# Optimization experiments

Measured on AMD Instinct MI355X. Metric: run time of the kernel, lower is better.

## Reference

```python
import jax, jax.numpy as jnp
from jax import lax
import numpy as np


def setup_inputs() -> dict:
    B, P, L, H, T = 4, 160, 128, 768, 9
    rng = np.random.default_rng(0)
    sent_length = rng.integers(L // 2, L + 1, size=B)
    sent_length[0] = L  # ensure max length equals L (pad_packed total_length)
    p2w = np.zeros((B, L, P), dtype=bool)
    for bi in range(B):
        pos = 1  # skip [CLS]
        for w in range(int(sent_length[bi])):
            n = 1 + int(rng.random() < 0.2)  # avg ~1.2 pieces per word
            if pos >= P - 1:
                break
            end = min(pos + n, P - 1)
            p2w[bi, w, pos:end] = True
            pos = end
    masks = np.arange(L)[None, :] < sent_length[:, None]
    labels = rng.integers(0, T, size=(B, L))
    key = jax.random.key(0)
    k1, k2, k3, k4, k5 = jax.random.split(key, 5)
    return {
        "bert_embs": jax.random.normal(k1, (B, P, H), jnp.float32),
        "pieces2word": jnp.asarray(p2w),
        "masks": jnp.asarray(masks),
        "labels": jnp.asarray(labels, jnp.int32),
        "sent_length": jnp.asarray(sent_length, jnp.int32),
        "W": jax.random.normal(k2, (H, T), jnp.float32) * 0.02,
        "b": jnp.zeros((T,), jnp.float32),
        "start_transitions": jax.random.uniform(k3, (T,), jnp.float32, -0.1, 0.1),
        "end_transitions": jax.random.uniform(k4, (T,), jnp.float32, -0.1, 0.1),
        "transitions": jax.random.uniform(k5, (T, T), jnp.float32, -0.1, 0.1),
    }


def crf_log_likelihood(emissions, tags, mask, start_t, end_t, trans):
    # torchcrf CRF forward (batch_first): log p(tags | emissions)
    B, L, T = emissions.shape
    maskf = mask.astype(emissions.dtype)
    barange = jnp.arange(B)
    # numerator: score of the gold tag sequence
    first_tags = tags[:, 0]
    num0 = start_t[first_tags] + emissions[barange, 0, first_tags]

    def num_step(s, inp):
        em_t, tp, tc, m = inp  # em_t: (B,T)
        return s + (trans[tp, tc] + em_t[barange, tc]) * m, None

    num, _ = lax.scan(
        num_step, num0,
        (emissions[:, 1:].transpose(1, 0, 2), tags[:, :-1].T, tags[:, 1:].T, maskf[:, 1:].T),
    )
    last_idx = jnp.sum(mask.astype(jnp.int32), axis=1) - 1
    num = num + end_t[tags[barange, last_idx]]
    # denominator: forward algorithm (log partition)
    alpha0 = start_t[None, :] + emissions[:, 0]  # (B,T)

    def den_step(a, inp):
        em_t, m = inp
        nxt = jax.nn.logsumexp(a[:, :, None] + trans[None, :, :] + em_t[:, None, :], axis=1)
        return jnp.where(m[:, None], nxt, a), None

    alpha, _ = lax.scan(den_step, alpha0, (emissions[:, 1:].transpose(1, 0, 2), mask[:, 1:].T))
    den = jax.nn.logsumexp(alpha + end_t[None, :], axis=1)
    return num - den


def reference(bert_embs, pieces2word, masks, labels, sent_length, W, b,
              start_transitions, end_transitions, transitions):
    min_value = lax.stop_gradient(jnp.min(bert_embs))  # .item() in torch detaches
    # expand + masked_fill + max over pieces: (B, L, P, H) -> (B, L, H)
    expanded = jnp.where(pieces2word[:, :, :, None], bert_embs[:, None, :, :], min_value)
    word_reps = jnp.max(expanded, axis=2)
    # pack_padded/pad_packed zeroes positions beyond sent_length
    word_reps = word_reps * masks[:, :, None].astype(word_reps.dtype)
    logits = word_reps @ W + b  # (B, L, T)
    llh = crf_log_likelihood(logits, labels, masks, start_transitions, end_transitions, transitions)
    loss = -jnp.sum(llh)  # module returns -1 * crf(...) (reduction='sum')
    return (loss, logits)
```

## Files before the change

kernel.cpp:

```cpp
#include <hip/hip_runtime.h>

#define NB 4
#define NP 160
#define NL 128
#define NH 768
#define NT 9
#define NBLK (NB * NL)
#define L2E 1.4426950408889634f
#define LN2 0.6931471805599453f

struct WS {
    float lg[NBLK * NT];
    float part[NBLK];
    int   empty[NBLK];
};

__device__ __forceinline__ float rdlane(float v, int p) {
    return __int_as_float(__builtin_amdgcn_readlane(__float_as_int(v), p));
}

__device__ __forceinline__ float dpp_add(float x) {
    float t;
#define STEP(ctrl, rmask, bc) \
    t = __int_as_float(__builtin_amdgcn_update_dpp(0, __float_as_int(x), ctrl, rmask, 0xf, bc)); \
    x += t;
    STEP(0x111, 0xf, true) STEP(0x112, 0xf, true) STEP(0x114, 0xf, true) STEP(0x118, 0xf, true)
    STEP(0x142, 0xa, false) STEP(0x143, 0xc, false)
#undef STEP
    return x;
}

__device__ __forceinline__ float dpp_fmin(float x) {
    float t;
#define STEP(ctrl, rmask) \
    t = __int_as_float(__builtin_amdgcn_update_dpp(__float_as_int(x), __float_as_int(x), ctrl, rmask, 0xf, false)); \
    x = fminf(x, t);
    STEP(0x111, 0xf) STEP(0x112, 0xf) STEP(0x114, 0xf) STEP(0x118, 0xf)
    STEP(0x142, 0xa) STEP(0x143, 0xc)
#undef STEP
    return x;
}

__device__ __forceinline__ float exp2v(float x) {
    float r; asm("v_exp_f32 %0, %1" : "=v"(r) : "v"(x)); return r;
}
__device__ __forceinline__ float log2v(float x) {
    float r; asm("v_log_f32 %0, %1" : "=v"(r) : "v"(x)); return r;
}

__global__ __launch_bounds__(256) void klogits(
    const float* __restrict__ embs, const void* __restrict__ p2w,
    const void* __restrict__ masks, const float* __restrict__ W,
    const float* __restrict__ bias, float* __restrict__ out_logits, WS* __restrict__ ws)
{
    const int bl = blockIdx.x;
    const int b  = bl / NL;
    const int tid = threadIdx.x;
    const int w = tid >> 6, lane = tid & 63;

    __shared__ float wrsh[NH];
    __shared__ int   plist[NP];
    __shared__ int   cnt;
    __shared__ int   isint_sh;
    __shared__ float wmin[4];

    const float4* e4 = (const float4*)(embs + bl * 960);
    float4 mv4 = (tid < 240) ? e4[tid] : make_float4(3.0e38f, 3.0e38f, 3.0e38f, 3.0e38f);
    unsigned char pb = 0;
    if (tid < NP) pb = ((const unsigned char*)p2w)[bl * NP + tid];
    const unsigned char mkb = ((const unsigned char*)masks)[bl];

    if (tid == 0) { isint_sh = (((const unsigned*)masks)[0] <= 1u); cnt = 0; }
    __syncthreads();
    const int is_int = isint_sh;

    int have = 0;
    if (tid < NP) have = is_int ? (((const int*)p2w)[bl * NP + tid] != 0) : (pb != 0);
    if (have) plist[atomicAdd(&cnt, 1)] = tid;

    float m = fminf(fminf(mv4.x, mv4.y), fminf(mv4.z, mv4.w));
    m = dpp_fmin(m);
    if (lane == 63) wmin[w] = m;

    const int mk = is_int ? (((const int*)masks)[bl] != 0) : (mkb != 0);
    __syncthreads();
    if (tid == 0) ws->part[bl] = fminf(fminf(wmin[0], wmin[1]), fminf(wmin[2], wmin[3]));

    const int nc = cnt;
    if (nc == 0) {
        if (tid == 0) ws->empty[bl] = mk ? 1 : 0;
        if (tid < NT) { float v = bias[tid]; out_logits[bl * NT + tid] = v; ws->lg[bl * NT + tid] = v; }
        return;
    }
    if (tid == 0) ws->empty[bl] = 0;

    #pragma unroll
    for (int k = 0; k < 3; k++) {
        int h = tid + k * 256;
        float wr = -3.0e38f;
        for (int i = 0; i < nc; i++)
            wr = fmaxf(wr, embs[(b * NP + plist[i]) * NH + h]);
        wrsh[h] = mk ? wr : 0.f;
    }
    __syncthreads();

    for (int t = w; t < NT; t += 4) {
        float acc = 0.f;
        #pragma unroll
        for (int j = 0; j < 12; j++) acc += wrsh[lane + j * 64] * W[(lane + j * 64) * NT + t];
        acc = dpp_add(acc);
        if (lane == 63) {
            float v = acc + bias[t];
            out_logits[bl * NT + t] = v;
            ws->lg[bl * NT + t]     = v;
        }
    }
}

__global__ __launch_bounds__(256) void kcrf(
    const int* __restrict__ labels, const int* __restrict__ sentlen,
    const float* __restrict__ W, const float* __restrict__ bias,
    const float* __restrict__ start_t, const float* __restrict__ end_t,
    const float* __restrict__ trans, WS* __restrict__ ws, float* __restrict__ out)
{
    __shared__ float em_s[NB * NL * NT + 16];
    __shared__ float trs[NT * NT];
    __shared__ int   lab_s[NB * NL];
    __shared__ float llh[NB];
    __shared__ float colsum[NT];
    __shared__ float wmin[4];

    const int tid  = threadIdx.x;
    const int w    = tid >> 6;
    const int lane = tid & 63;

    const float4* s4 = (const float4*)ws->lg;
    float4 lgv[4];
    #pragma unroll
    for (int r = 0; r < 4; r++) lgv[r] = s4[tid + r * 256];
    float4 lgt = (tid < 128) ? s4[tid + 1024] : make_float4(0, 0, 0, 0);
    int4  labv = (tid < 128) ? ((const int4*)labels)[tid] : make_int4(0, 0, 0, 0);
    float pmv  = fminf(ws->part[tid], ws->part[tid + 256]);
    float trv  = (tid < NT * NT) ? trans[tid] : 0.f;

    float4* d4 = (float4*)em_s;
    #pragma unroll
    for (int r = 0; r < 4; r++) d4[tid + r * 256] = lgv[r];
    if (tid < 128) d4[tid + 1024] = lgt;
    if (tid < 128) ((int4*)lab_s)[tid] = labv;
    if (tid < NT * NT) trs[tid] = trv * L2E;

    {
        float mv = dpp_fmin(pmv);
        if (lane == 63) wmin[w] = mv;
    }
    for (int t = w; t < NT; t += 4) {
        float s = 0.f;
        #pragma unroll
        for (int j = 0; j < 12; j++) s += W[(lane + j * 64) * NT + t];
        s = dpp_add(s);
        if (lane == 63) colsum[t] = s;
    }
    __syncthreads();
    const float minv = fminf(fminf(wmin[0], wmin[1]), fminf(wmin[2], wmin[3]));

    for (int r = tid; r < NBLK; r += 256) {
        if (ws->empty[r]) {
            #pragma unroll
            for (int t = 0; t < NT; t++) {
                float v = fmaf(minv, colsum[t], bias[t]);
                em_s[r * NT + t]    = v;
                out[1 + r * NT + t] = v;
            }
        }
    }
    __syncthreads();

    const int b   = w;
    const int c   = (lane < NT) ? lane : 0;
    const int len = sentlen[b];
    const float* em  = em_s + b * NL * NT;
    const int*   lab = lab_s + b * NL;

    float nsum = 0.f;
    for (int i = 1 + lane; i < len; i += 64) {
        int tp = lab[i - 1], tc = lab[i];
        nsum = fmaf(em[i * NT + tc], L2E, nsum + trs[tp * NT + tc]);
    }
    nsum = dpp_add(nsum);
    const float nsum_all = rdlane(nsum, 63);
    __syncthreads();

    float tcol[NT];
    #pragma unroll
    for (int p = 0; p < NT; p++) tcol[p] = trs[p * NT + c];

    float a    = fmaf(em[c], L2E, start_t[c] * L2E);
    float em_c = em[NT + c];
    for (int i = 1; i < len; i++) {
        float em_nx = em[(i + 1) * NT + c];
        float v0 = rdlane(a, 0) + tcol[0];
        float e[8];
        #pragma unroll
        for (int p = 1; p < NT; p++) {
            float d = (rdlane(a, p) + tcol[p]) - v0;
            e[p - 1] = exp2v(d);
        }
        float s = 1.0f + (((e[0] + e[1]) + (e[2] + e[3])) + ((e[4] + e[5]) + (e[6] + e[7])));
        float lg = log2v(s);
        a = fmaf(em_c, L2E, v0 + lg);
        em_c = em_nx;
    }

    float xv = a + end_t[c] * L2E;
    if (lane == 0) {
        float dv[NT];
        #pragma unroll
        for (int p = 0; p < NT; p++) dv[p] = rdlane(xv, p);
        float mx = fmaxf(fmaxf(fmaxf(dv[0], dv[1]), dv[2]),
                         fmaxf(fmaxf(fmaxf(dv[3], dv[4]), dv[5]),
                               fmaxf(fmaxf(dv[6], dv[7]), dv[8])));
        float s = 0.f;
        #pragma unroll
        for (int p = 0; p < NT; p++) s += exp2v(dv[p] - mx);
        float den = mx + log2v(s);
        int   t0  = lab[0];
        float num = fmaf(em[t0], L2E, nsum_all + start_t[t0] * L2E + end_t[lab[len - 1]] * L2E);
        llh[b] = (num - den) * LN2;
    }
    __syncthreads();
    if (tid == 0) out[0] = -(llh[0] + llh[1] + llh[2] + llh[3]);
}

extern "C" void kernel_launch(void* const* d_in, const int* in_sizes, int n_in,
                              void* d_out, int out_size, void* d_ws, size_t ws_size,
                              hipStream_t stream) {
    const float* embs    = (const float*)d_in[0];
    const void*  p2w     = d_in[1];
    const void*  masks   = d_in[2];
    const int*   labels  = (const int*)d_in[3];
    const int*   sentlen = (const int*)d_in[4];
    const float* W       = (const float*)d_in[5];
    const float* bias    = (const float*)d_in[6];
    const float* start_t = (const float*)d_in[7];
    const float* end_t   = (const float*)d_in[8];
    const float* trans   = (const float*)d_in[9];

    float* out = (float*)d_out;
    WS*    ws  = (WS*)d_ws;

    klogits<<<NBLK, 256, 0, stream>>>(embs, p2w, masks, W, bias, out + 1, ws);
    kcrf<<<1, 256, 0, stream>>>(labels, sentlen, W, bias, start_t, end_t, trans, ws, out);
}
```

Before: 34.07 us.

## Shorten CRF forward critical path and keep word max in registers

klogits now has every wavefront compute the piece max for all 768 hidden dims in registers, which removes the shared-memory staging and a barrier but repeats the max work in each wave. The mask is applied as a scale on the dot product instead. kcrf runs with 512 threads to load its inputs in fewer rounds, and the forward recursion is reformulated relative to tag 0. This lets the exp of the tag-0 transition be precomputed and the subtraction step be removed from the serial loop, with the absolute offset accumulated separately. The aim is to shorten the latency-bound per-timestep chain.

```diff
diff --git a/kernel.cpp b/kernel.cpp
--- a/kernel.cpp
+++ b/kernel.cpp
@@ -58,7 +58,6 @@
     const int tid = threadIdx.x;
     const int w = tid >> 6, lane = tid & 63;
 
-    __shared__ float wrsh[NH];
     __shared__ int   plist[NP];
     __shared__ int   cnt;
     __shared__ int   isint_sh;
@@ -94,30 +93,30 @@
     }
     if (tid == 0) ws->empty[bl] = 0;
 
+    float wr[12];
     #pragma unroll
-    for (int k = 0; k < 3; k++) {
-        int h = tid + k * 256;
-        float wr = -3.0e38f;
-        for (int i = 0; i < nc; i++)
-            wr = fmaxf(wr, embs[(b * NP + plist[i]) * NH + h]);
-        wrsh[h] = mk ? wr : 0.f;
-    }
-    __syncthreads();
+    for (int j = 0; j < 12; j++) wr[j] = -3.0e38f;
+    for (int i = 0; i < nc; i++) {
+        const float* er = embs + (b * NP + plist[i]) * NH;
+        #pragma unroll
+        for (int j = 0; j < 12; j++) wr[j] = fmaxf(wr[j], er[lane + j * 64]);
+    }
+    const float mkf = mk ? 1.0f : 0.0f;
 
     for (int t = w; t < NT; t += 4) {
         float acc = 0.f;
         #pragma unroll
-        for (int j = 0; j < 12; j++) acc += wrsh[lane + j * 64] * W[(lane + j * 64) * NT + t];
+        for (int j = 0; j < 12; j++) acc += wr[j] * W[(lane + j * 64) * NT + t];
         acc = dpp_add(acc);
         if (lane == 63) {
-            float v = acc + bias[t];
+            float v = fmaf(mkf, acc, bias[t]);
             out_logits[bl * NT + t] = v;
             ws->lg[bl * NT + t]     = v;
         }
     }
 }
 
-__global__ __launch_bounds__(256) void kcrf(
+__global__ __launch_bounds__(512) void kcrf(
     const int* __restrict__ labels, const int* __restrict__ sentlen,
     const float* __restrict__ W, const float* __restrict__ bias,
     const float* __restrict__ start_t, const float* __restrict__ end_t,
@@ -128,25 +127,24 @@
     __shared__ int   lab_s[NB * NL];
     __shared__ float llh[NB];
     __shared__ float colsum[NT];
-    __shared__ float wmin[4];
+    __shared__ float wmin[8];
 
     const int tid  = threadIdx.x;
     const int w    = tid >> 6;
     const int lane = tid & 63;
 
     const float4* s4 = (const float4*)ws->lg;
-    float4 lgv[4];
-    #pragma unroll
-    for (int r = 0; r < 4; r++) lgv[r] = s4[tid + r * 256];
-    float4 lgt = (tid < 128) ? s4[tid + 1024] : make_float4(0, 0, 0, 0);
+    float4 lgA = s4[tid];
+    float4 lgB = s4[tid + 512];
+    float4 lgC = (tid < 128) ? s4[tid + 1024] : make_float4(0, 0, 0, 0);
     int4  labv = (tid < 128) ? ((const int4*)labels)[tid] : make_int4(0, 0, 0, 0);
-    float pmv  = fminf(ws->part[tid], ws->part[tid + 256]);
+    float pmv  = ws->part[tid];
     float trv  = (tid < NT * NT) ? trans[tid] : 0.f;
 
     float4* d4 = (float4*)em_s;
-    #pragma unroll
-    for (int r = 0; r < 4; r++) d4[tid + r * 256] = lgv[r];
-    if (tid < 128) d4[tid + 1024] = lgt;
+    d4[tid]       = lgA;
+    d4[tid + 512] = lgB;
+    if (tid < 128) d4[tid + 1024] = lgC;
     if (tid < 128) ((int4*)lab_s)[tid] = labv;
     if (tid < NT * NT) trs[tid] = trv * L2E;
 
@@ -154,17 +152,20 @@
         float mv = dpp_fmin(pmv);
         if (lane == 63) wmin[w] = mv;
     }
-    for (int t = w; t < NT; t += 4) {
-        float s = 0.f;
-        #pragma unroll
-        for (int j = 0; j < 12; j++) s += W[(lane + j * 64) * NT + t];
-        s = dpp_add(s);
-        if (lane == 63) colsum[t] = s;
-    }
-    __syncthreads();
-    const float minv = fminf(fminf(wmin[0], wmin[1]), fminf(wmin[2], wmin[3]));
-
-    for (int r = tid; r < NBLK; r += 256) {
+    if (w < 4) {
+        for (int t = w; t < NT; t += 4) {
+            float s = 0.f;
+            #pragma unroll
+            for (int j = 0; j < 12; j++) s += W[(lane + j * 64) * NT + t];
+            s = dpp_add(s);
+            if (lane == 63) colsum[t] = s;
+        }
+    }
+    __syncthreads();
+    const float minv = fminf(fminf(fminf(wmin[0], wmin[1]), fminf(wmin[2], wmin[3])),
+                             fminf(fminf(wmin[4], wmin[5]), fminf(wmin[6], wmin[7])));
+
+    for (int r = tid; r < NBLK; r += 512) {
         if (ws->empty[r]) {
             #pragma unroll
             for (int t = 0; t < NT; t++) {
@@ -176,57 +177,72 @@
     }
     __syncthreads();
 
-    const int b   = w;
-    const int c   = (lane < NT) ? lane : 0;
-    const int len = sentlen[b];
-    const float* em  = em_s + b * NL * NT;
-    const int*   lab = lab_s + b * NL;
-
-    float nsum = 0.f;
-    for (int i = 1 + lane; i < len; i += 64) {
-        int tp = lab[i - 1], tc = lab[i];
-        nsum = fmaf(em[i * NT + tc], L2E, nsum + trs[tp * NT + tc]);
-    }
-    nsum = dpp_add(nsum);
-    const float nsum_all = rdlane(nsum, 63);
-    __syncthreads();
-
-    float tcol[NT];
-    #pragma unroll
-    for (int p = 0; p < NT; p++) tcol[p] = trs[p * NT + c];
-
-    float a    = fmaf(em[c], L2E, start_t[c] * L2E);
-    float em_c = em[NT + c];
-    for (int i = 1; i < len; i++) {
-        float em_nx = em[(i + 1) * NT + c];
-        float v0 = rdlane(a, 0) + tcol[0];
-        float e[8];
+    if (w < 4) {
+        const int b   = w;
+        const int c   = (lane < NT) ? lane : 0;
+        const int len = sentlen[b];
+        const float* em  = em_s + b * NL * NT;
+        const int*   lab = lab_s + b * NL;
+
+        float nsum = 0.f;
+        for (int i = 1 + lane; i < len; i += 64) {
+            int tp = lab[i - 1], tc = lab[i];
+            nsum = fmaf(em[i * NT + tc], L2E, nsum + trs[tp * NT + tc]);
+        }
+        nsum = dpp_add(nsum);
+        const float nsum_all = rdlane(nsum, 63);
+
+        float tcol[NT];
         #pragma unroll
-        for (int p = 1; p < NT; p++) {
-            float d = (rdlane(a, p) + tcol[p]) - v0;
-            e[p - 1] = exp2v(d);
-        }
-        float s = 1.0f + (((e[0] + e[1]) + (e[2] + e[3])) + ((e[4] + e[5]) + (e[6] + e[7])));
-        float lg = log2v(s);
-        a = fmaf(em_c, L2E, v0 + lg);
-        em_c = em_nx;
-    }
-
-    float xv = a + end_t[c] * L2E;
-    if (lane == 0) {
-        float dv[NT];
-        #pragma unroll
-        for (int p = 0; p < NT; p++) dv[p] = rdlane(xv, p);
-        float mx = fmaxf(fmaxf(fmaxf(dv[0], dv[1]), dv[2]),
-                         fmaxf(fmaxf(fmaxf(dv[3], dv[4]), dv[5]),
-                               fmaxf(fmaxf(dv[6], dv[7]), dv[8])));
-        float s = 0.f;
-        #pragma unroll
-        for (int p = 0; p < NT; p++) s += exp2v(dv[p] - mx);
-        float den = mx + log2v(s);
-        int   t0  = lab[0];
-        float num = fmaf(em[t0], L2E, nsum_all + start_t[t0] * L2E + end_t[lab[len - 1]] * L2E);
-        llh[b] = (num - den) * LN2;
+        for (int p = 0; p < NT; p++) tcol[p] = trs[p * NT + c];
+        const float ecol0 = exp2v(tcol[0]);
+
+        float vini = fmaf(em[c], L2E, start_t[c] * L2E);
+        float rv0  = rdlane(vini, 0);
+        float wrel = vini - rv0;
+        float a0abs = rv0;
+        float r1 = rdlane(wrel, 1), r2 = rdlane(wrel, 2), r3 = rdlane(wrel, 3);
+        float r4 = rdlane(wrel, 4), r5 = rdlane(wrel, 5), r6 = rdlane(wrel, 6);
+        float r7 = rdlane(wrel, 7), r8 = rdlane(wrel, 8);
+
+        float em_c = em[NT + c];
+        for (int i = 1; i < len; i++) {
+            float em_nx = em[(i + 1) * NT + c];
+            float e1 = exp2v(r1 + tcol[1]);
+            float e2 = exp2v(r2 + tcol[2]);
+            float e3 = exp2v(r3 + tcol[3]);
+            float e4 = exp2v(r4 + tcol[4]);
+            float e5 = exp2v(r5 + tcol[5]);
+            float e6 = exp2v(r6 + tcol[6]);
+            float e7 = exp2v(r7 + tcol[7]);
+            float e8 = exp2v(r8 + tcol[8]);
+            float s = (((ecol0 + e1) + (e2 + e3)) + ((e4 + e5) + (e6 + e7))) + e8;
+            float v = fmaf(em_c, L2E, log2v(s));
+            float nv0 = rdlane(v, 0);
+            wrel = v - nv0;
+            r1 = rdlane(wrel, 1); r2 = rdlane(wrel, 2); r3 = rdlane(wrel, 3);
+            r4 = rdlane(wrel, 4); r5 = rdlane(wrel, 5); r6 = rdlane(wrel, 6);
+            r7 = rdlane(wrel, 7); r8 = rdlane(wrel, 8);
+            a0abs += nv0;
+            em_c = em_nx;
+        }
+
+        float xv = wrel + end_t[c] * L2E;
+        if (lane == 0) {
+            float dv[NT];
+            #pragma unroll
+            for (int p = 0; p < NT; p++) dv[p] = rdlane(xv, p);
+            float mx = fmaxf(fmaxf(fmaxf(dv[0], dv[1]), dv[2]),
+                             fmaxf(fmaxf(fmaxf(dv[3], dv[4]), dv[5]),
+                                   fmaxf(fmaxf(dv[6], dv[7]), dv[8])));
+            float s = 0.f;
+            #pragma unroll
+            for (int p = 0; p < NT; p++) s += exp2v(dv[p] - mx);
+            float den = a0abs + mx + log2v(s);
+            int   t0  = lab[0];
+            float num = fmaf(em[t0], L2E, nsum_all + start_t[t0] * L2E + end_t[lab[len - 1]] * L2E);
+            llh[b] = (num - den) * LN2;
+        }
     }
     __syncthreads();
     if (tid == 0) out[0] = -(llh[0] + llh[1] + llh[2] + llh[3]);
@@ -250,5 +266,5 @@
     WS*    ws  = (WS*)d_ws;
 
     klogits<<<NBLK, 256, 0, stream>>>(embs, p2w, masks, W, bias, out + 1, ws);
-    kcrf<<<1, 256, 0, stream>>>(labels, sentlen, W, bias, start_t, end_t, trans, ws, out);
-}
+    kcrf<<<1, 512, 0, stream>>>(labels, sentlen, W, bias, start_t, end_t, trans, ws, out);
+}
```

Result: faster. 29.57 us (median of 2 runs) (-13.2%).
